# Kernel tuning notes

Hardware: AMD Instinct MI355X
Metric: run time of the kernel (lower is better)

## Reference

```python
import jax, jax.numpy as jnp
import numpy as np

WH, WW = 8, 8          # window size
NH = 8                 # num heads
ED = 256               # embed dim
HD = ED // NH          # head dim
SCALE = HD ** -0.5


def setup_inputs() -> dict:
    key = jax.random.key(0)
    k1, k2, k3, k4 = jax.random.split(key, 4)
    x = jax.random.normal(k1, (8, ED, 128, 128), dtype=jnp.float32)
    w_qkv = jax.random.normal(k2, (3 * ED, ED), dtype=jnp.float32) * (ED ** -0.5)
    w_out = jax.random.normal(k3, (ED, ED), dtype=jnp.float32) * (ED ** -0.5)
    b_out = jax.random.normal(k4, (ED,), dtype=jnp.float32) * 0.01
    return {"x": x, "w_qkv": w_qkv, "w_out": w_out, "b_out": b_out}


def reference(x, w_qkv, w_out, b_out):
    # x: [B, C, H, W] (NCHW) -> [B, H, W, C]
    x = jnp.transpose(x, (0, 2, 3, 1))
    B, H, W, C = x.shape
    pad_h = (WH - H % WH) % WH
    pad_w = (WW - W % WW) % WW
    x = jnp.pad(x, ((0, 0), (0, pad_h), (0, pad_w), (0, 0)))
    Hp, Wp = H + pad_h, W + pad_w
    nh, nw = Hp // WH, Wp // WW
    N = WH * WW
    # window partition -> [B*nh*nw, N, C]
    xw = x.reshape(B, nh, WH, nw, WW, C).transpose(0, 1, 3, 2, 4, 5).reshape(-1, N, C)
    # qkv projection (no bias): [nW, N, 3, NH, HD]
    qkv = (xw @ w_qkv.T).reshape(-1, N, 3, NH, HD)
    q, k, v = qkv[:, :, 0], qkv[:, :, 1], qkv[:, :, 2]  # [nW, N, NH, HD]
    # NOTE: faithful to source — attention across the HEADS axis per token
    attn = jnp.einsum('wnhd,wngd->wnhg', q, k) * SCALE  # [nW, N, NH, NH]
    attn = jax.nn.softmax(attn, axis=-1)
    out = jnp.einsum('wnhg,wngd->wnhd', attn, v)        # [nW, N, NH, HD]
    # torch: transpose(1,2).reshape(-1, N, C)
    out = out.transpose(0, 2, 1, 3).reshape(-1, N, C)
    out = out @ w_out.T + b_out
    # window merge
    out = out.reshape(B, nh, nw, WH, WW, C).transpose(0, 1, 3, 2, 4, 5).reshape(B, Hp, Wp, C)
    out = out[:, :H, :W, :]
    # faithful final permute(0,3,2,1): [B, C, W, H]
    return jnp.transpose(out, (0, 3, 2, 1))
```

## Files before the change

### kernel.cpp

```cpp
#include <hip/hip_runtime.h>

#define SCALE 0.17677669529663687f

typedef __attribute__((ext_vector_type(8))) short bf16x8;
typedef __attribute__((ext_vector_type(4))) float f32x4;

__device__ __forceinline__ unsigned short f2bf(float f) {
    unsigned u = __float_as_uint(f);
    u += 0x7FFFu + ((u >> 16) & 1u);
    return (unsigned short)(u >> 16);
}
__device__ __forceinline__ float bf2f(unsigned short s) {
    return __uint_as_float(((unsigned)s) << 16);
}
__device__ __forceinline__ unsigned pk2c(float a, float b) {
    return (unsigned)f2bf(a) | ((unsigned)f2bf(b) << 16);
}

__global__ __launch_bounds__(256) void wconv_kernel(
        const float* __restrict__ w_qkv, const float* __restrict__ w_out,
        unsigned short* __restrict__ wq, unsigned short* __restrict__ wo) {
    int idx = blockIdx.x * 256 + threadIdx.x;
    if (idx < 196608) wq[idx] = f2bf(w_qkv[idx]);
    else if (idx < 262144) wo[idx - 196608] = f2bf(w_out[idx - 196608]);
}

__global__ __launch_bounds__(512, 4) void qkv_gemm_kernel(
        const float* __restrict__ x, const unsigned short* __restrict__ wq,
        unsigned short* __restrict__ qkv_ws) {
    __shared__ unsigned char lds[65536];
    const int tid  = threadIdx.x;
    const int tb   = blockIdx.x << 6;
    const int b    = tb >> 14;
    const int hw0  = tb & 16383;
    const float* xb = x + (size_t)b * 4194304 + hw0;
    const int tok  = tid & 63;
    const int wave = tid >> 6;

    #pragma unroll
    for (int cg = 0; cg < 4; ++cg) {
        const int c0 = wave * 32 + cg * 8;
        float f[8];
        #pragma unroll
        for (int e = 0; e < 8; ++e) f[e] = xb[(size_t)(c0 + e) * 16384 + tok];
        unsigned u0 = pk2c(f[0], f[1]), u1 = pk2c(f[2], f[3]);
        unsigned u2 = pk2c(f[4], f[5]), u3 = pk2c(f[6], f[7]);
        const int slot = (c0 >> 3) ^ (tok & 7);
        *(uint4*)(lds + tok * 512 + (slot << 4)) = make_uint4(u0, u1, u2, u3);
    }
    __syncthreads();

    const int lane = tid & 63;
    const int lrow = lane & 15, lk = lane >> 4;
    const int j0w = wave * 32;

    for (int nb = 0; nb < 3; ++nb) {
        f32x4 acc[4][2];
        #pragma unroll
        for (int mt = 0; mt < 4; ++mt)
            #pragma unroll
            for (int nt = 0; nt < 2; ++nt)
                acc[mt][nt] = (f32x4){0.f, 0.f, 0.f, 0.f};
        #pragma unroll
        for (int k = 0; k < 8; ++k) {
            bf16x8 a[4], bb[2];
            #pragma unroll
            for (int mt = 0; mt < 4; ++mt) {
                int t = mt * 16 + lrow;
                int slot = (k * 4 + lk) ^ (t & 7);
                a[mt] = *(const bf16x8*)(lds + t * 512 + (slot << 4));
            }
            #pragma unroll
            for (int nt = 0; nt < 2; ++nt) {
                int j = nb * 256 + j0w + nt * 16 + lrow;
                bb[nt] = *(const bf16x8*)((const unsigned char*)wq + (size_t)j * 512 + k * 64 + lk * 16);
            }
            #pragma unroll
            for (int mt = 0; mt < 4; ++mt)
                #pragma unroll
                for (int nt = 0; nt < 2; ++nt)
                    acc[mt][nt] = __builtin_amdgcn_mfma_f32_16x16x32_bf16(a[mt], bb[nt], acc[mt][nt], 0, 0, 0);
        }
        #pragma unroll
        for (int mt = 0; mt < 4; ++mt)
            #pragma unroll
            for (int nt = 0; nt < 2; ++nt)
                #pragma unroll
                for (int i = 0; i < 4; ++i) {
                    int t = mt * 16 + lk * 4 + i;
                    int ch = j0w + nt * 16 + lrow;
                    int slot = (ch >> 3) ^ (t & 7);
                    *(unsigned short*)(lds + 32768 + t * 512 + (slot << 4) + (ch & 7) * 2) = f2bf(acc[mt][nt][i]);
                }
        __syncthreads();
        #pragma unroll
        for (int it = 0; it < 4; ++it) {
            int idx = it * 512 + tid;
            int t = idx >> 5, c = idx & 31;
            int slot = c ^ (t & 7);
            bf16x8 vch = *(const bf16x8*)(lds + 32768 + t * 512 + (slot << 4));
            *(bf16x8*)(qkv_ws + (size_t)(tb + t) * 768 + nb * 256 + c * 8) = vch;
        }
        __syncthreads();
    }
}

__global__ __launch_bounds__(256, 4) void attn_kernel(
        const unsigned short* __restrict__ qkv_ws, unsigned short* __restrict__ o_ws) {
    const int tid = threadIdx.x;
    const int tok = (blockIdx.x << 4) + (tid >> 4);
    const int h   = (tid >> 1) & 7;
    const int hf  = tid & 1;
    const unsigned short* row = qkv_ws + (size_t)tok * 768;

    float q[16];
    #pragma unroll
    for (int jj = 0; jj < 2; ++jj) {
        bf16x8 v = *(const bf16x8*)(row + h * 32 + hf * 16 + jj * 8);
        #pragma unroll
        for (int e = 0; e < 8; ++e) q[jj * 8 + e] = bf2f((unsigned short)v[e]);
    }
    float dots[8];
    #pragma unroll
    for (int g = 0; g < 8; ++g) {
        float acc = 0.f;
        #pragma unroll
        for (int jj = 0; jj < 2; ++jj) {
            bf16x8 v = *(const bf16x8*)(row + 256 + g * 32 + hf * 16 + jj * 8);
            #pragma unroll
            for (int e = 0; e < 8; ++e) acc += q[jj * 8 + e] * bf2f((unsigned short)v[e]);
        }
        dots[g] = acc;
    }
    #pragma unroll
    for (int g = 0; g < 8; ++g)
        dots[g] = (dots[g] + __shfl_xor(dots[g], 1, 64)) * SCALE;
    float mx = dots[0];
    #pragma unroll
    for (int g = 1; g < 8; ++g) mx = fmaxf(mx, dots[g]);
    float sum = 0.f;
    #pragma unroll
    for (int g = 0; g < 8; ++g) { dots[g] = __expf(dots[g] - mx); sum += dots[g]; }
    const float inv = 1.f / sum;
    float o[16];
    #pragma unroll
    for (int d = 0; d < 16; ++d) o[d] = 0.f;
    #pragma unroll
    for (int g = 0; g < 8; ++g) {
        const float p = dots[g] * inv;
        #pragma unroll
        for (int jj = 0; jj < 2; ++jj) {
            bf16x8 v = *(const bf16x8*)(row + 512 + g * 32 + hf * 16 + jj * 8);
            #pragma unroll
            for (int e = 0; e < 8; ++e) o[jj * 8 + e] += p * bf2f((unsigned short)v[e]);
        }
    }
    const int bb2 = tok >> 14, rem = tok & 16383;
    const int himg = rem >> 7, wimg = rem & 127;
    const int ih = himg >> 3, r = himg & 7;
    const int iw = wimg >> 3, s = wimg & 7;
    const int win = (bb2 << 8) + (ih << 4) + iw;
    unsigned short* dst = o_ws + ((size_t)win * 64 + h * 8 + r) * 256 + s * 32 + hf * 16;
    #pragma unroll
    for (int jj = 0; jj < 2; ++jj) {
        uint4 v = make_uint4(pk2c(o[jj * 8 + 0], o[jj * 8 + 1]), pk2c(o[jj * 8 + 2], o[jj * 8 + 3]),
                             pk2c(o[jj * 8 + 4], o[jj * 8 + 5]), pk2c(o[jj * 8 + 6], o[jj * 8 + 7]));
        *(uint4*)(dst + jj * 8) = v;
    }
}

__global__ __launch_bounds__(512, 6) void outproj_kernel(
        const unsigned short* __restrict__ o_ws, const unsigned short* __restrict__ wo,
        const float* __restrict__ b_out, float* __restrict__ out) {
    __shared__ unsigned char lds[32768];
    const int tid = threadIdx.x;
    const int bid = blockIdx.x;
    const int b  = bid >> 8;
    const int ih = (bid >> 4) & 15;
    const int iw = bid & 15;

    {
        const unsigned char* src = (const unsigned char*)(o_ws + (size_t)bid * 16384);
        #pragma unroll
        for (int it = 0; it < 4; ++it) {
            int q = it * 512 + tid;
            int np = q >> 5;
            int slot = (q & 31) ^ (np & 7);
            *(bf16x8*)(lds + np * 512 + (slot << 4)) = *(const bf16x8*)(src + q * 16);
        }
    }
    __syncthreads();

    const int lane = tid & 63;
    const int wave = tid >> 6;
    const int lrow = lane & 15;
    const int lk   = lane >> 4;
    const int j0 = wave * 32;

    f32x4 acc[4][2];
    #pragma unroll
    for (int mt = 0; mt < 4; ++mt)
        #pragma unroll
        for (int nt = 0; nt < 2; ++nt)
            acc[mt][nt] = (f32x4){0.f, 0.f, 0.f, 0.f};
    #pragma unroll
    for (int k = 0; k < 8; ++k) {
        bf16x8 a[4], bb[2];
        #pragma unroll
        for (int mt = 0; mt < 4; ++mt) {
            int t = mt * 16 + lrow;
            int slot = (k * 4 + lk) ^ (t & 7);
            a[mt] = *(const bf16x8*)(lds + t * 512 + (slot << 4));
        }
        #pragma unroll
        for (int nt = 0; nt < 2; ++nt) {
            int j = j0 + nt * 16 + lrow;
            bb[nt] = *(const bf16x8*)((const unsigned char*)wo + (size_t)j * 512 + k * 64 + lk * 16);
        }
        #pragma unroll
        for (int mt = 0; mt < 4; ++mt)
            #pragma unroll
            for (int nt = 0; nt < 2; ++nt)
                acc[mt][nt] = __builtin_amdgcn_mfma_f32_16x16x32_bf16(a[mt], bb[nt], acc[mt][nt], 0, 0, 0);
    }
    float bias[2];
    #pragma unroll
    for (int nt = 0; nt < 2; ++nt) bias[nt] = b_out[j0 + nt * 16 + lrow];
    __syncthreads();

    const size_t obase = ((size_t)b * 256) * 16384 + (size_t)(iw * 8) * 128 + ih * 8;
    #pragma unroll
    for (int half = 0; half < 2; ++half) {
        if ((wave >> 2) == half) {
            int jl = (wave & 3) * 32;
            #pragma unroll
            for (int mt = 0; mt < 4; ++mt)
                #pragma unroll
                for (int nt = 0; nt < 2; ++nt)
                    #pragma unroll
                    for (int i = 0; i < 4; ++i) {
                        int t = mt * 16 + lk * 4 + i;
                        int el = jl + nt * 16 + lrow;
                        int sl = (el >> 2) ^ (t & 7);
                        *(float*)(lds + t * 512 + (sl << 4) + (el & 3) * 4) = acc[mt][nt][i] + bias[nt];
                    }
        }
        __syncthreads();
        #pragma unroll
        for (int it = 0; it < 2; ++it) {
            int idx = it * 512 + tid;
            int el = idx >> 3, sp = idx & 7;
            float vals[8];
            #pragma unroll
            for (int rp = 0; rp < 8; ++rp) {
                int t = rp * 8 + sp;
                int sl = (el >> 2) ^ (t & 7);
                vals[rp] = *(const float*)(lds + t * 512 + (sl << 4) + (el & 3) * 4);
            }
            float* po = out + obase + (size_t)(half * 128 + el) * 16384 + sp * 128;
            *(float4*)po       = make_float4(vals[0], vals[1], vals[2], vals[3]);
            *(float4*)(po + 4) = make_float4(vals[4], vals[5], vals[6], vals[7]);
        }
        __syncthreads();
    }
}

extern "C" void kernel_launch(void* const* d_in, const int* in_sizes, int n_in,
                              void* d_out, int out_size, void* d_ws, size_t ws_size,
                              hipStream_t stream) {
    const float* x     = (const float*)d_in[0];
    const float* w_qkv = (const float*)d_in[1];
    const float* w_out = (const float*)d_in[2];
    const float* b_out = (const float*)d_in[3];
    float* out = (float*)d_out;

    const size_t QKV_BYTES = 201326592;
    const size_t O_BYTES   = 67108864;

    unsigned short* qkv_ws = (unsigned short*)d_ws;
    unsigned short* o_ws   = (unsigned short*)((char*)d_ws + QKV_BYTES);
    unsigned short* wq     = (unsigned short*)((char*)d_ws + QKV_BYTES + O_BYTES);
    unsigned short* wo     = wq + 196608;

    wconv_kernel<<<dim3(1024), dim3(256), 0, stream>>>(w_qkv, w_out, wq, wo);
    qkv_gemm_kernel<<<dim3(2048), dim3(512), 0, stream>>>(x, wq, qkv_ws);
    attn_kernel<<<dim3(8192), dim3(256), 0, stream>>>(qkv_ws, o_ws);
    outproj_kernel<<<dim3(2048), dim3(512), 0, stream>>>(o_ws, wo, b_out, out);
}
```

Baseline: 281.4 us.

## Fuse attention into out-projection kernel and shrink QKV GEMM LDS staging

Measured after the change: 304.1 us. 8.1% more time.

```diff
diff --git a/kernel.cpp b/kernel.cpp
--- a/kernel.cpp
+++ b/kernel.cpp
@@ -25,10 +25,10 @@
     else if (idx < 262144) wo[idx - 196608] = f2bf(w_out[idx - 196608]);
 }
 
-__global__ __launch_bounds__(512, 4) void qkv_gemm_kernel(
+__global__ __launch_bounds__(512, 6) void qkv_gemm_kernel(
         const float* __restrict__ x, const unsigned short* __restrict__ wq,
         unsigned short* __restrict__ qkv_ws) {
-    __shared__ unsigned char lds[65536];
+    __shared__ unsigned char lds[49152];
     const int tid  = threadIdx.x;
     const int tb   = blockIdx.x << 6;
     const int b    = tb >> 14;
@@ -82,95 +82,36 @@
                     acc[mt][nt] = __builtin_amdgcn_mfma_f32_16x16x32_bf16(a[mt], bb[nt], acc[mt][nt], 0, 0, 0);
         }
         #pragma unroll
-        for (int mt = 0; mt < 4; ++mt)
-            #pragma unroll
-            for (int nt = 0; nt < 2; ++nt)
-                #pragma unroll
-                for (int i = 0; i < 4; ++i) {
-                    int t = mt * 16 + lk * 4 + i;
-                    int ch = j0w + nt * 16 + lrow;
-                    int slot = (ch >> 3) ^ (t & 7);
-                    *(unsigned short*)(lds + 32768 + t * 512 + (slot << 4) + (ch & 7) * 2) = f2bf(acc[mt][nt][i]);
-                }
-        __syncthreads();
-        #pragma unroll
-        for (int it = 0; it < 4; ++it) {
-            int idx = it * 512 + tid;
-            int t = idx >> 5, c = idx & 31;
-            int slot = c ^ (t & 7);
-            bf16x8 vch = *(const bf16x8*)(lds + 32768 + t * 512 + (slot << 4));
-            *(bf16x8*)(qkv_ws + (size_t)(tb + t) * 768 + nb * 256 + c * 8) = vch;
-        }
-        __syncthreads();
-    }
-}
-
-__global__ __launch_bounds__(256, 4) void attn_kernel(
-        const unsigned short* __restrict__ qkv_ws, unsigned short* __restrict__ o_ws) {
-    const int tid = threadIdx.x;
-    const int tok = (blockIdx.x << 4) + (tid >> 4);
-    const int h   = (tid >> 1) & 7;
-    const int hf  = tid & 1;
-    const unsigned short* row = qkv_ws + (size_t)tok * 768;
-
-    float q[16];
-    #pragma unroll
-    for (int jj = 0; jj < 2; ++jj) {
-        bf16x8 v = *(const bf16x8*)(row + h * 32 + hf * 16 + jj * 8);
-        #pragma unroll
-        for (int e = 0; e < 8; ++e) q[jj * 8 + e] = bf2f((unsigned short)v[e]);
-    }
-    float dots[8];
-    #pragma unroll
-    for (int g = 0; g < 8; ++g) {
-        float acc = 0.f;
-        #pragma unroll
-        for (int jj = 0; jj < 2; ++jj) {
-            bf16x8 v = *(const bf16x8*)(row + 256 + g * 32 + hf * 16 + jj * 8);
-            #pragma unroll
-            for (int e = 0; e < 8; ++e) acc += q[jj * 8 + e] * bf2f((unsigned short)v[e]);
-        }
-        dots[g] = acc;
-    }
-    #pragma unroll
-    for (int g = 0; g < 8; ++g)
-        dots[g] = (dots[g] + __shfl_xor(dots[g], 1, 64)) * SCALE;
-    float mx = dots[0];
-    #pragma unroll
-    for (int g = 1; g < 8; ++g) mx = fmaxf(mx, dots[g]);
-    float sum = 0.f;
-    #pragma unroll
-    for (int g = 0; g < 8; ++g) { dots[g] = __expf(dots[g] - mx); sum += dots[g]; }
-    const float inv = 1.f / sum;
-    float o[16];
-    #pragma unroll
-    for (int d = 0; d < 16; ++d) o[d] = 0.f;
-    #pragma unroll
-    for (int g = 0; g < 8; ++g) {
-        const float p = dots[g] * inv;
-        #pragma unroll
-        for (int jj = 0; jj < 2; ++jj) {
-            bf16x8 v = *(const bf16x8*)(row + 512 + g * 32 + hf * 16 + jj * 8);
-            #pragma unroll
-            for (int e = 0; e < 8; ++e) o[jj * 8 + e] += p * bf2f((unsigned short)v[e]);
-        }
-    }
-    const int bb2 = tok >> 14, rem = tok & 16383;
-    const int himg = rem >> 7, wimg = rem & 127;
-    const int ih = himg >> 3, r = himg & 7;
-    const int iw = wimg >> 3, s = wimg & 7;
-    const int win = (bb2 << 8) + (ih << 4) + iw;
-    unsigned short* dst = o_ws + ((size_t)win * 64 + h * 8 + r) * 256 + s * 32 + hf * 16;
-    #pragma unroll
-    for (int jj = 0; jj < 2; ++jj) {
-        uint4 v = make_uint4(pk2c(o[jj * 8 + 0], o[jj * 8 + 1]), pk2c(o[jj * 8 + 2], o[jj * 8 + 3]),
-                             pk2c(o[jj * 8 + 4], o[jj * 8 + 5]), pk2c(o[jj * 8 + 6], o[jj * 8 + 7]));
-        *(uint4*)(dst + jj * 8) = v;
-    }
-}
-
-__global__ __launch_bounds__(512, 6) void outproj_kernel(
-        const unsigned short* __restrict__ o_ws, const unsigned short* __restrict__ wo,
+        for (int th = 0; th < 2; ++th) {
+            __syncthreads();
+            #pragma unroll
+            for (int mh = 0; mh < 2; ++mh) {
+                const int mt = th * 2 + mh;
+                #pragma unroll
+                for (int nt = 0; nt < 2; ++nt)
+                    #pragma unroll
+                    for (int i = 0; i < 4; ++i) {
+                        int tl = mh * 16 + lk * 4 + i;
+                        int ch = j0w + nt * 16 + lrow;
+                        int slot = (ch >> 3) ^ (tl & 7);
+                        *(unsigned short*)(lds + 32768 + tl * 512 + (slot << 4) + (ch & 7) * 2) = f2bf(acc[mt][nt][i]);
+                    }
+            }
+            __syncthreads();
+            #pragma unroll
+            for (int it = 0; it < 2; ++it) {
+                int idx = it * 512 + tid;
+                int tl = idx >> 5, c = idx & 31;
+                int slot = c ^ (tl & 7);
+                bf16x8 vch = *(const bf16x8*)(lds + 32768 + tl * 512 + (slot << 4));
+                *(bf16x8*)(qkv_ws + (size_t)(tb + th * 32 + tl) * 768 + nb * 256 + c * 8) = vch;
+            }
+        }
+    }
+}
+
+__global__ __launch_bounds__(512, 6) void attn_outproj_kernel(
+        const unsigned short* __restrict__ qkv_ws, const unsigned short* __restrict__ wo,
         const float* __restrict__ b_out, float* __restrict__ out) {
     __shared__ unsigned char lds[32768];
     const int tid = threadIdx.x;
@@ -178,15 +119,66 @@
     const int b  = bid >> 8;
     const int ih = (bid >> 4) & 15;
     const int iw = bid & 15;
-
-    {
-        const unsigned char* src = (const unsigned char*)(o_ws + (size_t)bid * 16384);
-        #pragma unroll
-        for (int it = 0; it < 4; ++it) {
-            int q = it * 512 + tid;
-            int np = q >> 5;
-            int slot = (q & 31) ^ (np & 7);
-            *(bf16x8*)(lds + np * 512 + (slot << 4)) = *(const bf16x8*)(src + q * 16);
+    const size_t tokbase = (size_t)b * 16384 + (size_t)(ih * 8) * 128 + iw * 8;
+
+    #pragma unroll
+    for (int task = 0; task < 2; ++task) {
+        const int tt = task * 512 + tid;
+        const int t  = tt >> 4;
+        const int h  = (tt >> 1) & 7;
+        const int hf = tt & 1;
+        const int r = t >> 3, s = t & 7;
+        const unsigned short* row = qkv_ws + (tokbase + r * 128 + s) * 768;
+
+        float q[16];
+        #pragma unroll
+        for (int jj = 0; jj < 2; ++jj) {
+            bf16x8 v = *(const bf16x8*)(row + h * 32 + hf * 16 + jj * 8);
+            #pragma unroll
+            for (int e = 0; e < 8; ++e) q[jj * 8 + e] = bf2f((unsigned short)v[e]);
+        }
+        float dots[8];
+        #pragma unroll
+        for (int g = 0; g < 8; ++g) {
+            float acc = 0.f;
+            #pragma unroll
+            for (int jj = 0; jj < 2; ++jj) {
+                bf16x8 v = *(const bf16x8*)(row + 256 + g * 32 + hf * 16 + jj * 8);
+                #pragma unroll
+                for (int e = 0; e < 8; ++e) acc += q[jj * 8 + e] * bf2f((unsigned short)v[e]);
+            }
+            dots[g] = acc;
+        }
+        #pragma unroll
+        for (int g = 0; g < 8; ++g)
+            dots[g] = (dots[g] + __shfl_xor(dots[g], 1, 64)) * SCALE;
+        float mx = dots[0];
+        #pragma unroll
+        for (int g = 1; g < 8; ++g) mx = fmaxf(mx, dots[g]);
+        float sum = 0.f;
+        #pragma unroll
+        for (int g = 0; g < 8; ++g) { dots[g] = __expf(dots[g] - mx); sum += dots[g]; }
+        const float inv = 1.f / sum;
+        float o[16];
+        #pragma unroll
+        for (int d = 0; d < 16; ++d) o[d] = 0.f;
+        #pragma unroll
+        for (int g = 0; g < 8; ++g) {
+            const float p = dots[g] * inv;
+            #pragma unroll
+            for (int jj = 0; jj < 2; ++jj) {
+                bf16x8 v = *(const bf16x8*)(row + 512 + g * 32 + hf * 16 + jj * 8);
+                #pragma unroll
+                for (int e = 0; e < 8; ++e) o[jj * 8 + e] += p * bf2f((unsigned short)v[e]);
+            }
+        }
+        const int np = h * 8 + r;
+        #pragma unroll
+        for (int jj = 0; jj < 2; ++jj) {
+            const int c = s * 4 + hf * 2 + jj;
+            uint4 v = make_uint4(pk2c(o[jj * 8 + 0], o[jj * 8 + 1]), pk2c(o[jj * 8 + 2], o[jj * 8 + 3]),
+                                 pk2c(o[jj * 8 + 4], o[jj * 8 + 5]), pk2c(o[jj * 8 + 6], o[jj * 8 + 7]));
+            *(uint4*)(lds + np * 512 + ((c ^ (np & 7)) << 4)) = v;
         }
     }
     __syncthreads();
@@ -275,15 +267,12 @@
     float* out = (float*)d_out;
 
     const size_t QKV_BYTES = 201326592;
-    const size_t O_BYTES   = 67108864;
 
     unsigned short* qkv_ws = (unsigned short*)d_ws;
-    unsigned short* o_ws   = (unsigned short*)((char*)d_ws + QKV_BYTES);
-    unsigned short* wq     = (unsigned short*)((char*)d_ws + QKV_BYTES + O_BYTES);
+    unsigned short* wq     = (unsigned short*)((char*)d_ws + QKV_BYTES);
     unsigned short* wo     = wq + 196608;
 
     wconv_kernel<<<dim3(1024), dim3(256), 0, stream>>>(w_qkv, w_out, wq, wo);
     qkv_gemm_kernel<<<dim3(2048), dim3(512), 0, stream>>>(x, wq, qkv_ws);
-    attn_kernel<<<dim3(8192), dim3(256), 0, stream>>>(qkv_ws, o_ws);
-    outproj_kernel<<<dim3(2048), dim3(512), 0, stream>>>(o_ws, wo, b_out, out);
-}
+    attn_outproj_kernel<<<dim3(2048), dim3(512), 0, stream>>>(qkv_ws, wo, b_out, out);
+}
```

## Cut QKV GEMM LDS footprint, batch x loads, pack paired bf16 epilogue stores

Applied to the files above, without the earlier changes.

Measured after the change: 287.7 us. +2.2%, slower.

```diff
diff --git a/kernel.cpp b/kernel.cpp
--- a/kernel.cpp
+++ b/kernel.cpp
@@ -28,7 +28,7 @@
 __global__ __launch_bounds__(512, 4) void qkv_gemm_kernel(
         const float* __restrict__ x, const unsigned short* __restrict__ wq,
         unsigned short* __restrict__ qkv_ws) {
-    __shared__ unsigned char lds[65536];
+    __shared__ unsigned char lds[49152];
     const int tid  = threadIdx.x;
     const int tb   = blockIdx.x << 6;
     const int b    = tb >> 14;
@@ -37,14 +37,17 @@
     const int tok  = tid & 63;
     const int wave = tid >> 6;
 
+    float f[32];
+    #pragma unroll
+    for (int cg = 0; cg < 4; ++cg)
+        #pragma unroll
+        for (int e = 0; e < 8; ++e)
+            f[cg * 8 + e] = xb[(size_t)(wave * 32 + cg * 8 + e) * 16384 + tok];
     #pragma unroll
     for (int cg = 0; cg < 4; ++cg) {
         const int c0 = wave * 32 + cg * 8;
-        float f[8];
-        #pragma unroll
-        for (int e = 0; e < 8; ++e) f[e] = xb[(size_t)(c0 + e) * 16384 + tok];
-        unsigned u0 = pk2c(f[0], f[1]), u1 = pk2c(f[2], f[3]);
-        unsigned u2 = pk2c(f[4], f[5]), u3 = pk2c(f[6], f[7]);
+        unsigned u0 = pk2c(f[cg*8+0], f[cg*8+1]), u1 = pk2c(f[cg*8+2], f[cg*8+3]);
+        unsigned u2 = pk2c(f[cg*8+4], f[cg*8+5]), u3 = pk2c(f[cg*8+6], f[cg*8+7]);
         const int slot = (c0 >> 3) ^ (tok & 7);
         *(uint4*)(lds + tok * 512 + (slot << 4)) = make_uint4(u0, u1, u2, u3);
     }
@@ -72,7 +75,7 @@
             }
             #pragma unroll
             for (int nt = 0; nt < 2; ++nt) {
-                int j = nb * 256 + j0w + nt * 16 + lrow;
+                int j = nb * 256 + j0w + lrow * 2 + nt;
                 bb[nt] = *(const bf16x8*)((const unsigned char*)wq + (size_t)j * 512 + k * 64 + lk * 16);
             }
             #pragma unroll
@@ -82,26 +85,30 @@
                     acc[mt][nt] = __builtin_amdgcn_mfma_f32_16x16x32_bf16(a[mt], bb[nt], acc[mt][nt], 0, 0, 0);
         }
         #pragma unroll
-        for (int mt = 0; mt < 4; ++mt)
-            #pragma unroll
-            for (int nt = 0; nt < 2; ++nt)
+        for (int th = 0; th < 2; ++th) {
+            __syncthreads();
+            #pragma unroll
+            for (int mh = 0; mh < 2; ++mh) {
+                const int mt = th * 2 + mh;
                 #pragma unroll
                 for (int i = 0; i < 4; ++i) {
-                    int t = mt * 16 + lk * 4 + i;
-                    int ch = j0w + nt * 16 + lrow;
-                    int slot = (ch >> 3) ^ (t & 7);
-                    *(unsigned short*)(lds + 32768 + t * 512 + (slot << 4) + (ch & 7) * 2) = f2bf(acc[mt][nt][i]);
+                    int tl = mh * 16 + lk * 4 + i;
+                    int ch = j0w + lrow * 2;
+                    int slot = (ch >> 3) ^ (tl & 7);
+                    unsigned pr = pk2c(acc[mt][0][i], acc[mt][1][i]);
+                    *(unsigned*)(lds + 32768 + tl * 512 + (slot << 4) + (ch & 7) * 2) = pr;
                 }
-        __syncthreads();
-        #pragma unroll
-        for (int it = 0; it < 4; ++it) {
-            int idx = it * 512 + tid;
-            int t = idx >> 5, c = idx & 31;
-            int slot = c ^ (t & 7);
-            bf16x8 vch = *(const bf16x8*)(lds + 32768 + t * 512 + (slot << 4));
-            *(bf16x8*)(qkv_ws + (size_t)(tb + t) * 768 + nb * 256 + c * 8) = vch;
-        }
-        __syncthreads();
+            }
+            __syncthreads();
+            #pragma unroll
+            for (int it = 0; it < 2; ++it) {
+                int idx = it * 512 + tid;
+                int tl = idx >> 5, c = idx & 31;
+                int slot = c ^ (tl & 7);
+                bf16x8 vch = *(const bf16x8*)(lds + 32768 + tl * 512 + (slot << 4));
+                *(bf16x8*)(qkv_ws + (size_t)(tb + th * 32 + tl) * 768 + nb * 256 + c * 8) = vch;
+            }
+        }
     }
 }
 
```
